# Performance work log

Measured on AMD Instinct MI355X. Metric: run time of the kernel, lower is better.

## Reference

```python
import jax, jax.numpy as jnp
import numpy as np

B, S, D, H, HID = 4, 1024, 1024, 16, 4096
DK = D // H
EPS = 1e-6


def _ln(x):
    # LayerNorm without affine, eps=1e-6
    mu = jnp.mean(x, axis=-1, keepdims=True)
    var = jnp.var(x, axis=-1, keepdims=True)
    return (x - mu) / jnp.sqrt(var + EPS)


def _lin(x, W, b):
    # torch Linear convention: W is [out, in]
    y = jnp.einsum('...i,oi->...o', x, W)
    return y + b if b is not None else y


def setup_inputs() -> dict:
    key = jax.random.key(0)
    ks = jax.random.split(key, 16)
    sc = lambda fan_in: 1.0 / np.sqrt(fan_in)
    inp = {
        'x': jax.random.normal(ks[0], (B, S, D), jnp.float32),
        'cond': jax.random.normal(ks[1], (B, 1, D), jnp.float32),
        'Wq': jax.random.normal(ks[2], (D, D), jnp.float32) * sc(D),
        'bq': jnp.zeros((D,), jnp.float32),
        'Wk': jax.random.normal(ks[3], (D, D), jnp.float32) * sc(D),
        'bk': jnp.zeros((D,), jnp.float32),
        'Wv': jax.random.normal(ks[4], (D, D), jnp.float32) * sc(D),
        'bv': jnp.zeros((D,), jnp.float32),
        'Wo': jax.random.normal(ks[5], (D, D), jnp.float32) * sc(D),
        'bo': jnp.zeros((D,), jnp.float32),
        'W1': jax.random.normal(ks[6], (HID, D), jnp.float32) * sc(D),
        'b1': jnp.zeros((HID,), jnp.float32),
        'W2': jax.random.normal(ks[7], (D, HID), jnp.float32) * sc(HID),
        'b2': jnp.zeros((D,), jnp.float32),
        'Wada': jax.random.normal(ks[8], (6 * D, D), jnp.float32) * sc(D),
        'bada': jnp.zeros((6 * D,), jnp.float32),
    }
    return inp


def reference(x, cond, Wq, bq, Wk, bk, Wv, bv, Wo, bo, W1, b1, W2, b2, Wada, bada):
    # adaLN modulation: SiLU -> Linear -> chunk 6 along last dim
    mod = _lin(jax.nn.silu(cond), Wada, bada)  # [B,1,6D]
    gama1, beta1, alpha1, gama2, beta2, alpha2 = jnp.split(mod, 6, axis=-1)

    # attention branch
    residual = x
    h = _ln(x) * (1.0 + beta1) + gama1  # modulate(shift=gama1, scale=beta1)
    q = _lin(h, Wq, bq).reshape(B, S, H, DK)
    k = _lin(h, Wk, bk).reshape(B, S, H, DK)
    v = _lin(h, Wv, bv).reshape(B, S, H, DK)
    scores = jnp.einsum('bqhd,bkhd->bhqk', q, k) / jnp.sqrt(jnp.float32(DK))
    probs = jax.nn.softmax(scores, axis=-1)
    attn = jnp.einsum('bhqk,bkhd->bqhd', probs, v).reshape(B, S, D)
    attn = _lin(attn, Wo, bo)
    x = residual + alpha1 * attn

    # MLP branch
    residual = x
    h = _ln(x) * (1.0 + beta2) + gama2
    h = _lin(h, W1, b1)
    h = jax.nn.gelu(h, approximate=False)  # torch nn.GELU default (erf)
    h = _lin(h, W2, b2)
    return residual + alpha2 * h
```

## Files before the change

### kernel.cpp

```cpp
#include <hip/hip_runtime.h>
#include <cstdint>

typedef __bf16 bf16_t;
typedef __bf16 bf16x4 __attribute__((ext_vector_type(4)));
typedef __bf16 bf16x8 __attribute__((ext_vector_type(8)));
typedef float f32x4 __attribute__((ext_vector_type(4)));

#define B_ 4
#define S_ 1024
#define D_ 1024
#define HID_ 4096
#define MEG (1u << 20)

static const size_t OFF_WBF  = 0;
static const size_t OFF_BQKV = 25165824;
static const size_t OFF_MOD  = 25178112;
static const size_t OFF_H    = 25276416;
static const size_t OFF_QKV  = 33665024;
static const size_t OFF_VT   = 58830848;
static const size_t OFF_ATTN = 67219456;
static const size_t OFF_X1   = 75608064;
static const size_t OFF_PART = 92385280;
static const size_t OFF_MLPH = 159494144;

__device__ __forceinline__ void async_copy16(const bf16_t* g, bf16_t* l) {
  __builtin_amdgcn_global_load_lds(
      (__attribute__((address_space(1))) void*)(g),
      (__attribute__((address_space(3))) void*)(l), 16, 0, 0);
}

__global__ __launch_bounds__(256) void convert_pack(
    const float* __restrict__ Wq, const float* __restrict__ Wk,
    const float* __restrict__ Wv, const float* __restrict__ Wo,
    const float* __restrict__ W1, const float* __restrict__ W2,
    const float* __restrict__ bq, const float* __restrict__ bk,
    const float* __restrict__ bv, bf16_t* __restrict__ wbf,
    float* __restrict__ bqkv) {
  const int y = blockIdx.y;
  if (y == 6) {
    int i = blockIdx.x * 256 + threadIdx.x;
    if (i < 3072)
      bqkv[i] = i < 1024 ? bq[i] : (i < 2048 ? bk[i - 1024] : bv[i - 2048]);
    return;
  }
  const float* src; bf16_t* dst; int n;
  switch (y) {
    case 0: src = Wq; dst = wbf;           n = MEG;     break;
    case 1: src = Wk; dst = wbf + MEG;     n = MEG;     break;
    case 2: src = Wv; dst = wbf + 2*MEG;   n = MEG;     break;
    case 3: src = Wo; dst = wbf + 3*MEG;   n = MEG;     break;
    case 4: src = W1; dst = wbf + 4*MEG;   n = 4*MEG;   break;
    default: src = W2; dst = wbf + 8*MEG;  n = 4*MEG;   break;
  }
  int idx = (blockIdx.x * 256 + threadIdx.x) * 4;
  if (idx < n) {
    float4 v = *(const float4*)(src + idx);
    bf16x4 pk;
    pk.x = (__bf16)v.x; pk.y = (__bf16)v.y; pk.z = (__bf16)v.z; pk.w = (__bf16)v.w;
    *(bf16x4*)(dst + idx) = pk;
  }
}

__global__ __launch_bounds__(256) void ada_mod(
    const float* __restrict__ cond, const float* __restrict__ Wada,
    const float* __restrict__ bada, float* __restrict__ mod) {
  const int wave = threadIdx.x >> 6, lane = threadIdx.x & 63;
  const int o = blockIdx.x * 4 + wave;
  const float* wr = Wada + (size_t)o * D_;
  float a0 = 0.f, a1 = 0.f, a2 = 0.f, a3 = 0.f;
#pragma unroll
  for (int l = 0; l < 16; l++) {
    int i = l * 64 + lane;
    float w = wr[i];
    float c0 = cond[i], c1 = cond[1024 + i], c2 = cond[2048 + i], c3 = cond[3072 + i];
    a0 += w * (c0 / (1.0f + __expf(-c0)));
    a1 += w * (c1 / (1.0f + __expf(-c1)));
    a2 += w * (c2 / (1.0f + __expf(-c2)));
    a3 += w * (c3 / (1.0f + __expf(-c3)));
  }
#pragma unroll
  for (int offs = 32; offs; offs >>= 1) {
    a0 += __shfl_xor(a0, offs);
    a1 += __shfl_xor(a1, offs);
    a2 += __shfl_xor(a2, offs);
    a3 += __shfl_xor(a3, offs);
  }
  if (lane == 0) {
    float bb = bada[o];
    mod[o]          = a0 + bb;
    mod[6144 + o]   = a1 + bb;
    mod[12288 + o]  = a2 + bb;
    mod[18432 + o]  = a3 + bb;
  }
}

__global__ __launch_bounds__(256) void ln_modulate(
    const float* __restrict__ X, const float* __restrict__ mod,
    bf16_t* __restrict__ H, int goff) {
  const int row = blockIdx.x;
  const int b = row >> 10;
  const int t = threadIdx.x;
  const float* xr = X + (size_t)row * D_;
  float4 xv = *(const float4*)(xr + t * 4);
  float s = xv.x + xv.y + xv.z + xv.w;
  float q = xv.x*xv.x + xv.y*xv.y + xv.z*xv.z + xv.w*xv.w;
  const int wave = t >> 6, lane = t & 63;
#pragma unroll
  for (int offs = 32; offs; offs >>= 1) {
    s += __shfl_down(s, offs);
    q += __shfl_down(q, offs);
  }
  __shared__ float sb[4][2];
  if (lane == 0) { sb[wave][0] = s; sb[wave][1] = q; }
  __syncthreads();
  float st = sb[0][0] + sb[1][0] + sb[2][0] + sb[3][0];
  float qt = sb[0][1] + sb[1][1] + sb[2][1] + sb[3][1];
  float mu = st * (1.0f / D_);
  float var = qt * (1.0f / D_) - mu * mu;
  float rstd = rsqrtf(var + 1e-6f);
  const float* mb = mod + (size_t)b * 6144 + goff;
  const int c = t * 4;
  float4 gm = *(const float4*)(mb + c);
  float4 bt = *(const float4*)(mb + 1024 + c);
  bf16x4 pk;
  pk.x = (__bf16)((xv.x - mu) * rstd * (1.0f + bt.x) + gm.x);
  pk.y = (__bf16)((xv.y - mu) * rstd * (1.0f + bt.y) + gm.y);
  pk.z = (__bf16)((xv.z - mu) * rstd * (1.0f + bt.z) + gm.z);
  pk.w = (__bf16)((xv.w - mu) * rstd * (1.0f + bt.w) + gm.w);
  *(bf16x4*)(H + (size_t)row * D_ + c) = pk;
}

__global__ __launch_bounds__(256) void transpose_v(
    const bf16_t* __restrict__ qkv, bf16_t* __restrict__ vT) {
  __shared__ bf16_t tile[64][65];
  const int bh = blockIdx.y;
  const int b = bh >> 4, hh = bh & 15;
  const int s0 = blockIdx.x * 64;
  const int t = threadIdx.x;
  const int tx = t & 63, ty = t >> 6;
  const bf16_t* src = qkv + (size_t)b * S_ * 3072 + 2048 + hh * 64;
  for (int r = ty; r < 64; r += 4)
    tile[r][tx] = src[(size_t)(s0 + r) * 3072 + tx];
  __syncthreads();
  bf16_t* dst = vT + (size_t)bh * 64 * 1024;
  for (int r = ty; r < 64; r += 4)
    dst[(size_t)r * 1024 + s0 + tx] = tile[tx][r];
}

__global__ __launch_bounds__(512, 4) void flash_attn(
    const bf16_t* __restrict__ qkv, const bf16_t* __restrict__ vT,
    bf16_t* __restrict__ attn) {
  __shared__ __align__(16) bf16_t Ks[2][2][64 * 64];
  __shared__ __align__(16) bf16_t Vs[2][2][64 * 64];
  __shared__ __align__(16) bf16_t Ps[8][16 * 64];

  const int t = threadIdx.x;
  const int wave = t >> 6, lane = t & 63;
  const int lm = lane & 15, quad = lane >> 4;
  const int bh = blockIdx.y;
  const int b = bh >> 4, hh = bh & 15;
  const int s0 = blockIdx.x * 128;

  const bf16_t* qbase = qkv + (size_t)b * S_ * 3072 + hh * 64;
  const bf16_t* kbase = qbase + 1024;
  const bf16_t* vbase = vT + (size_t)bh * (64 * 1024);

  const int row0 = t >> 3;
  const int cg = (t & 7) ^ (row0 & 7);
  const int od = t * 8;

  async_copy16(qbase + (size_t)(s0 + row0) * 3072 + cg * 8, &Ks[1][0][od]);
  async_copy16(qbase + (size_t)(s0 + 64 + row0) * 3072 + cg * 8, &Ks[1][1][od]);
  async_copy16(kbase + (size_t)row0 * 3072 + cg * 8, &Ks[0][0][od]);
  async_copy16(kbase + (size_t)(64 + row0) * 3072 + cg * 8, &Ks[0][1][od]);
  async_copy16(vbase + (size_t)row0 * 1024 + cg * 8, &Vs[0][0][od]);
  async_copy16(vbase + (size_t)row0 * 1024 + 64 + cg * 8, &Vs[0][1][od]);
  __syncthreads();

  bf16x8 aq0, aq1;
  {
    const int rq = wave * 16 + lm;
    const int qh = rq >> 6, qr = rq & 63;
    const int rbq = lm & 7;
    aq0 = *(const bf16x8*)&Ks[1][qh][qr * 64 + (quad ^ rbq) * 8];
    aq1 = *(const bf16x8*)&Ks[1][qh][qr * 64 + ((4 + quad) ^ rbq) * 8];
  }
  __syncthreads();

  f32x4 accO[4] = {};
  float mrow[4], lsum[4];
#pragma unroll
  for (int r = 0; r < 4; r++) { mrow[r] = -1e30f; lsum[r] = 0.f; }

  const float SC = 0.18033688f;
  const int rb = lm & 7;
  bf16_t* Pw = Ps[wave];

  for (int tt = 0; tt < 8; ++tt) {
    const int cur = tt & 1;
    if (tt < 7) {
      const int nb = cur ^ 1;
      const size_t k0n = (size_t)(tt + 1) << 7;
      async_copy16(kbase + (k0n + row0) * 3072 + cg * 8, &Ks[nb][0][od]);
      async_copy16(kbase + (k0n + 64 + row0) * 3072 + cg * 8, &Ks[nb][1][od]);
      async_copy16(vbase + (size_t)row0 * 1024 + k0n + cg * 8, &Vs[nb][0][od]);
      async_copy16(vbase + (size_t)row0 * 1024 + k0n + 64 + cg * 8, &Vs[nb][1][od]);
    }

    f32x4 accS[8];
#pragma unroll
    for (int j = 0; j < 8; j++) accS[j] = (f32x4){0.f, 0.f, 0.f, 0.f};
    __builtin_amdgcn_s_setprio(1);
#pragma unroll
    for (int hf = 0; hf < 2; hf++) {
#pragma unroll
      for (int ni = 0; ni < 4; ni++) {
        const int rk = ni * 16 + lm;
        bf16x8 b0 = *(const bf16x8*)&Ks[cur][hf][rk * 64 + ((quad ^ rb)) * 8];
        bf16x8 b1 = *(const bf16x8*)&Ks[cur][hf][rk * 64 + (((4 + quad) ^ rb)) * 8];
        f32x4 a = accS[hf * 4 + ni];
        a = __builtin_amdgcn_mfma_f32_16x16x32_bf16(aq0, b0, a, 0, 0, 0);
        a = __builtin_amdgcn_mfma_f32_16x16x32_bf16(aq1, b1, a, 0, 0, 0);
        accS[hf * 4 + ni] = a;
      }
    }
    __builtin_amdgcn_s_setprio(0);

    float mx[4];
#pragma unroll
    for (int r = 0; r < 4; r++) {
      float m0 = fmaxf(fmaxf(accS[0][r], accS[1][r]), fmaxf(accS[2][r], accS[3][r]));
      float m1 = fmaxf(fmaxf(accS[4][r], accS[5][r]), fmaxf(accS[6][r], accS[7][r]));
      float m8 = fmaxf(m0, m1);
      m8 = fmaxf(m8, __shfl_xor(m8, 1));
      m8 = fmaxf(m8, __shfl_xor(m8, 2));
      m8 = fmaxf(m8, __shfl_xor(m8, 4));
      m8 = fmaxf(m8, __shfl_xor(m8, 8));
      mx[r] = m8 * SC;
    }
    bool ok = (mx[0] - mrow[0] <= 8.0f) && (mx[1] - mrow[1] <= 8.0f) &&
              (mx[2] - mrow[2] <= 8.0f) && (mx[3] - mrow[3] <= 8.0f);
    if (!__all(ok)) {
#pragma unroll
      for (int r = 0; r < 4; r++) {
        float mnew = fmaxf(mrow[r], mx[r]);
        float al = exp2f(mrow[r] - mnew);
        mrow[r] = mnew;
        lsum[r] *= al;
#pragma unroll
        for (int di = 0; di < 4; di++) accO[di][r] *= al;
      }
    }
#pragma unroll
    for (int r = 0; r < 4; r++) {
      float sum = 0.f;
#pragma unroll
      for (int j = 0; j < 8; j++) {
        float p = exp2f(accS[j][r] * SC - mrow[r]);
        accS[j][r] = p;
        sum += p;
      }
      lsum[r] += sum;
    }

#pragma unroll
    for (int hf = 0; hf < 2; hf++) {
#pragma unroll
      for (int jj = 0; jj < 4; jj++)
#pragma unroll
        for (int r = 0; r < 4; r++) {
          int prow = quad * 4 + r;
          int c = jj * 16 + lm;
          Pw[prow * 64 + (((c >> 3) ^ (prow & 7)) << 3) + (c & 7)] =
              (__bf16)accS[hf * 4 + jj][r];
        }
      __builtin_amdgcn_s_setprio(1);
#pragma unroll
      for (int loc = 0; loc < 2; loc++) {
        bf16x8 ap = *(const bf16x8*)&Pw[lm * 64 + (((loc * 4 + quad) ^ rb)) * 8];
#pragma unroll
        for (int di = 0; di < 4; di++) {
          const int rv = di * 16 + lm;
          bf16x8 vv = *(const bf16x8*)&Vs[cur][hf]
              [rv * 64 + (((loc * 4 + quad) ^ rb)) * 8];
          accO[di] = __builtin_amdgcn_mfma_f32_16x16x32_bf16(ap, vv, accO[di], 0, 0, 0);
        }
      }
      __builtin_amdgcn_s_setprio(0);
    }
    __syncthreads();
  }

#pragma unroll
  for (int r = 0; r < 4; r++) {
    float sv = lsum[r];
    sv += __shfl_xor(sv, 1);
    sv += __shfl_xor(sv, 2);
    sv += __shfl_xor(sv, 4);
    sv += __shfl_xor(sv, 8);
    lsum[r] = sv;
  }

#pragma unroll
  for (int r = 0; r < 4; r++) {
    float inv = 1.0f / lsum[r];
    int prow = quad * 4 + r;
#pragma unroll
    for (int di = 0; di < 4; di++) {
      int col = di * 16 + lm;
      int cph = (col >> 3) ^ (prow & 7);
      Pw[prow * 64 + cph * 8 + (col & 7)] = (__bf16)(accO[di][r] * inv);
    }
  }
  bf16_t* abase = attn + (size_t)b * S_ * 1024 +
                  (size_t)(s0 + wave * 16) * 1024 + hh * 64;
#pragma unroll
  for (int it = 0; it < 2; it++) {
    int slot = it * 64 + lane;
    int orow = slot >> 3;
    int gc = slot & 7;
    int cph = gc ^ (orow & 7);
    bf16x8 val = *(const bf16x8*)&Pw[orow * 64 + cph * 8];
    *(bf16x8*)(abase + (size_t)orow * 1024 + gc * 8) = val;
  }
}

template <int EPI>
__global__ __launch_bounds__(512) void gemm_bt(
    const bf16_t* __restrict__ A, int lda, long long sAz,
    const bf16_t* __restrict__ B, int ldb, long long sBz,
    void* __restrict__ Cv, int ldc, long long sCz,
    int M, int N, int K,
    const float* __restrict__ bias,
    float scale) {
  __shared__ __align__(16) bf16_t As[3][256 * 64];
  __shared__ __align__(16) bf16_t Bs[3][128 * 64];

  const int z = blockIdx.z;
  A += (size_t)z * sAz;
  B += (size_t)z * sBz;

  const int gx = gridDim.x;
  int d = blockIdx.x + gx * blockIdx.y;
  {
    const int cpx = (gx * gridDim.y) >> 3;
    int wg = (d & 7) * cpx + (d >> 3);
    const int by = wg / gx;
    const int bx = wg % gx;

    const int t = threadIdx.x;
    const int wave = t >> 6;
    const int lane = t & 63;
    const int lm = lane & 15;
    const int quad = lane >> 4;
    const int wr = wave >> 1;
    const int wc = wave & 1;

    const int m0 = by * 256;
    const int n0 = bx * 128;

    f32x4 acc[4][4] = {};

    const int srow = t >> 3;
    const int scg = (t & 7) ^ (srow & 7);
    const int sod = t * 8;
    const bf16_t* Ag = A + (size_t)(m0 + srow) * lda + scg * 8;
    const bf16_t* Bg = B + (size_t)(n0 + srow) * ldb + scg * 8;
    const size_t a64 = (size_t)64 * lda, a128 = (size_t)128 * lda,
                 a192 = (size_t)192 * lda, b64 = (size_t)64 * ldb;

#define STAGE6(buf, ko)                                      \
  async_copy16(Ag + (ko), &As[buf][sod]);                    \
  async_copy16(Ag + a64 + (ko), &As[buf][4096 + sod]);       \
  async_copy16(Ag + a128 + (ko), &As[buf][8192 + sod]);      \
  async_copy16(Ag + a192 + (ko), &As[buf][12288 + sod]);     \
  async_copy16(Bg + (ko), &Bs[buf][sod]);                    \
  async_copy16(Bg + b64 + (ko), &Bs[buf][4096 + sod]);

    const int niter = K >> 6;
    STAGE6(0, 0);
    STAGE6(1, 64);

    const int rbx = lm & 7;
    const int sl0 = (quad ^ rbx) * 8;
    const int sl1 = ((4 + quad) ^ rbx) * 8;
    const int arow = wr * 4096 + lm * 64;
    const int brow = wc * 4096 + lm * 64;

    int cur = 0;
    for (int it = 0; it < niter; ++it) {
      if (it + 1 < niter) {
        asm volatile("s_waitcnt vmcnt(6)\n\ts_barrier" ::: "memory");
      } else {
        asm volatile("s_waitcnt vmcnt(0)\n\ts_barrier" ::: "memory");
      }
      if (it + 2 < niter) {
        const int nb = (cur >= 1) ? cur - 1 : 2;
        const int ko = (it + 2) << 6;
        STAGE6(nb, ko);
      }
      bf16x8 af[4][2], bfr[4][2];
#pragma unroll
      for (int i = 0; i < 4; i++) {
        af[i][0] = *(const bf16x8*)&As[cur][arow + i * 1024 + sl0];
        af[i][1] = *(const bf16x8*)&As[cur][arow + i * 1024 + sl1];
        bfr[i][0] = *(const bf16x8*)&Bs[cur][brow + i * 1024 + sl0];
        bfr[i][1] = *(const bf16x8*)&Bs[cur][brow + i * 1024 + sl1];
      }
      __builtin_amdgcn_s_setprio(1);
#pragma unroll
      for (int ks = 0; ks < 2; ks++)
#pragma unroll
        for (int mi = 0; mi < 4; mi++)
#pragma unroll
          for (int ni = 0; ni < 4; ni++)
            acc[mi][ni] = __builtin_amdgcn_mfma_f32_16x16x32_bf16(
                af[mi][ks], bfr[ni][ks], acc[mi][ni], 0, 0, 0);
      __builtin_amdgcn_s_setprio(0);
      cur = (cur == 2) ? 0 : cur + 1;
    }
#undef STAGE6

    const size_t cz = (size_t)z * sCz;
#pragma unroll
    for (int mi = 0; mi < 4; mi++) {
#pragma unroll
      for (int ni = 0; ni < 4; ni++) {
#pragma unroll
        for (int r = 0; r < 4; r++) {
          int row = m0 + wr * 64 + mi * 16 + quad * 4 + r;
          int col = n0 + wc * 64 + ni * 16 + lm;
          float v = acc[mi][ni][r];
          size_t idx = cz + (size_t)row * ldc + col;
          if (EPI == 1) {
            ((float*)Cv)[idx] = v * scale;
          } else if (EPI == 0) {
            if (bias) v += bias[col];
            ((bf16_t*)Cv)[idx] = (__bf16)v;
          } else if (EPI == 3) {
            v += bias[col];
            float u = 1.5957691216f * (v + 0.044715f * v * v * v);
            float g = v / (1.0f + __expf(-u));
            ((bf16_t*)Cv)[idx] = (__bf16)g;
          }
        }
      }
    }
  }
}

__global__ __launch_bounds__(256) void reduce_ln(
    const float* __restrict__ part, const float* __restrict__ x,
    const float* __restrict__ bo, const float* __restrict__ mod,
    float* __restrict__ x1, bf16_t* __restrict__ h) {
  const int row = blockIdx.x;
  const int b = row >> 10;
  const int t = threadIdx.x;
  const int c = t * 4;
  const size_t idx = (size_t)row * 1024 + c;
  float4 p0 = *(const float4*)(part + idx);
  float4 p1 = *(const float4*)(part + 4194304 + idx);
  float4 bb = *(const float4*)(bo + c);
  float4 al = *(const float4*)(mod + (size_t)b * 6144 + 2048 + c);
  float4 xs = *(const float4*)(x + idx);
  float4 xv;
  xv.x = xs.x + al.x * (p0.x + p1.x + bb.x);
  xv.y = xs.y + al.y * (p0.y + p1.y + bb.y);
  xv.z = xs.z + al.z * (p0.z + p1.z + bb.z);
  xv.w = xs.w + al.w * (p0.w + p1.w + bb.w);
  *(float4*)(x1 + idx) = xv;

  float s = xv.x + xv.y + xv.z + xv.w;
  float q = xv.x*xv.x + xv.y*xv.y + xv.z*xv.z + xv.w*xv.w;
  const int wave = t >> 6, lane = t & 63;
#pragma unroll
  for (int offs = 32; offs; offs >>= 1) {
    s += __shfl_down(s, offs);
    q += __shfl_down(q, offs);
  }
  __shared__ float sb[4][2];
  if (lane == 0) { sb[wave][0] = s; sb[wave][1] = q; }
  __syncthreads();
  float st = sb[0][0] + sb[1][0] + sb[2][0] + sb[3][0];
  float qt = sb[0][1] + sb[1][1] + sb[2][1] + sb[3][1];
  float mu = st * (1.0f / D_);
  float var = qt * (1.0f / D_) - mu * mu;
  float rstd = rsqrtf(var + 1e-6f);
  const float* mb = mod + (size_t)b * 6144 + 3072;
  float4 gm = *(const float4*)(mb + c);
  float4 bt = *(const float4*)(mb + 1024 + c);
  bf16x4 pk;
  pk.x = (__bf16)((xv.x - mu) * rstd * (1.0f + bt.x) + gm.x);
  pk.y = (__bf16)((xv.y - mu) * rstd * (1.0f + bt.y) + gm.y);
  pk.z = (__bf16)((xv.z - mu) * rstd * (1.0f + bt.z) + gm.z);
  pk.w = (__bf16)((xv.w - mu) * rstd * (1.0f + bt.w) + gm.w);
  *(bf16x4*)(h + idx) = pk;
}

__global__ __launch_bounds__(256) void reduce_w2(
    const float* __restrict__ part, const float* __restrict__ x1,
    const float* __restrict__ b2, const float* __restrict__ mod,
    float* __restrict__ out) {
  const int idx = (blockIdx.x * 256 + threadIdx.x) * 4;
  const int col = idx & 1023;
  const int row = idx >> 10;
  const int b = row >> 10;
  float4 s0 = *(const float4*)(part + idx);
  float4 s1 = *(const float4*)(part + 4194304 + idx);
  float4 bb = *(const float4*)(b2 + col);
  float4 al = *(const float4*)(mod + (size_t)b * 6144 + 5120 + col);
  float4 rs = *(const float4*)(x1 + idx);
  float4 o;
  o.x = rs.x + al.x * (s0.x + s1.x + bb.x);
  o.y = rs.y + al.y * (s0.y + s1.y + bb.y);
  o.z = rs.z + al.z * (s0.z + s1.z + bb.z);
  o.w = rs.w + al.w * (s0.w + s1.w + bb.w);
  *(float4*)(out + idx) = o;
}

extern "C" void kernel_launch(void* const* d_in, const int* in_sizes, int n_in,
                              void* d_out, int out_size, void* d_ws, size_t ws_size,
                              hipStream_t stream) {
  (void)in_sizes; (void)n_in; (void)out_size; (void)ws_size;
  const float* x    = (const float*)d_in[0];
  const float* cond = (const float*)d_in[1];
  const float* Wq   = (const float*)d_in[2];
  const float* bq   = (const float*)d_in[3];
  const float* Wk   = (const float*)d_in[4];
  const float* bk   = (const float*)d_in[5];
  const float* Wv   = (const float*)d_in[6];
  const float* bv   = (const float*)d_in[7];
  const float* Wo   = (const float*)d_in[8];
  const float* bo   = (const float*)d_in[9];
  const float* W1   = (const float*)d_in[10];
  const float* b1   = (const float*)d_in[11];
  const float* W2   = (const float*)d_in[12];
  const float* b2   = (const float*)d_in[13];
  const float* Wada = (const float*)d_in[14];
  const float* bada = (const float*)d_in[15];

  uint8_t* ws = (uint8_t*)d_ws;
  bf16_t* wbf   = (bf16_t*)(ws + OFF_WBF);
  float*  bqkv  = (float*)(ws + OFF_BQKV);
  float*  mod   = (float*)(ws + OFF_MOD);
  bf16_t* h     = (bf16_t*)(ws + OFF_H);
  bf16_t* qkv   = (bf16_t*)(ws + OFF_QKV);
  bf16_t* vT    = (bf16_t*)(ws + OFF_VT);
  bf16_t* attn  = (bf16_t*)(ws + OFF_ATTN);
  float*  x1    = (float*)(ws + OFF_X1);
  float*  part  = (float*)(ws + OFF_PART);
  bf16_t* mlph  = (bf16_t*)(ws + OFF_MLPH);
  float* out = (float*)d_out;

  convert_pack<<<dim3(4096, 7, 1), 256, 0, stream>>>(Wq, Wk, Wv, Wo, W1, W2,
                                                     bq, bk, bv, wbf, bqkv);
  ada_mod<<<1536, 256, 0, stream>>>(cond, Wada, bada, mod);
  ln_modulate<<<4096, 256, 0, stream>>>(x, mod, h, 0);
  gemm_bt<0><<<dim3(24, 16, 1), 512, 0, stream>>>(
      h, 1024, 0, wbf, 1024, 0, qkv, 3072, 0, 4096, 3072, 1024,
      bqkv, 1.f);
  transpose_v<<<dim3(16, 64, 1), 256, 0, stream>>>(qkv, vT);
  flash_attn<<<dim3(8, 64, 1), 512, 0, stream>>>(qkv, vT, attn);

  gemm_bt<1><<<dim3(8, 16, 2), 512, 0, stream>>>(
      attn, 1024, 512, wbf + (size_t)3 * MEG, 1024, 512, part, 1024, 4194304,
      4096, 1024, 512, nullptr, 1.f);
  reduce_ln<<<4096, 256, 0, stream>>>(part, x, bo, mod, x1, h);

  gemm_bt<3><<<dim3(32, 16, 1), 512, 0, stream>>>(
      h, 1024, 0, wbf + (size_t)4 * MEG, 1024, 0, mlph, 4096, 0,
      4096, 4096, 1024, b1, 1.f);
  gemm_bt<1><<<dim3(8, 16, 2), 512, 0, stream>>>(
      mlph, 4096, 2048, wbf + (size_t)8 * MEG, 4096, 2048, part, 1024, 4194304,
      4096, 1024, 2048, nullptr, 1.f);
  reduce_w2<<<4096, 256, 0, stream>>>(part, x1, b2, mod, out);
}
```

Baseline: 412.5 us.

## Split GEMM main loop into two phases interleaving LDS reads, async copies and MFMAs

Each K-iteration of the bf16 GEMM main loop now runs in two halves. Each half reads part of the A fragments from LDS, issues half of the next-stage async global-to-LDS copies, and runs half of the MFMAs, with extra barriers between phases. The goal is to overlap global loads and LDS traffic with matrix-core work more finely, in a ping-pong style schedule. The cost is four barriers per iteration instead of one, and a possible change in register pressure.

```diff
diff --git a/kernel.cpp b/kernel.cpp
--- a/kernel.cpp
+++ b/kernel.cpp
@@ -390,32 +390,65 @@
     int cur = 0;
     for (int it = 0; it < niter; ++it) {
       if (it + 1 < niter) {
-        asm volatile("s_waitcnt vmcnt(6)\n\ts_barrier" ::: "memory");
+        asm volatile("s_waitcnt vmcnt(6)" ::: "memory");
       } else {
-        asm volatile("s_waitcnt vmcnt(0)\n\ts_barrier" ::: "memory");
-      }
-      if (it + 2 < niter) {
-        const int nb = (cur >= 1) ? cur - 1 : 2;
-        const int ko = (it + 2) << 6;
-        STAGE6(nb, ko);
-      }
-      bf16x8 af[4][2], bfr[4][2];
+        asm volatile("s_waitcnt vmcnt(0)" ::: "memory");
+      }
+      __builtin_amdgcn_s_barrier();
+      const int nb = (cur >= 1) ? cur - 1 : 2;
+      const int ko = (it + 2) << 6;
+      const bool st = (it + 2 < niter);
+
+      bf16x8 af0[2], af1[2], bfr[4][2];
+      af0[0] = *(const bf16x8*)&As[cur][arow + sl0];
+      af0[1] = *(const bf16x8*)&As[cur][arow + sl1];
+      af1[0] = *(const bf16x8*)&As[cur][arow + 1024 + sl0];
+      af1[1] = *(const bf16x8*)&As[cur][arow + 1024 + sl1];
 #pragma unroll
       for (int i = 0; i < 4; i++) {
-        af[i][0] = *(const bf16x8*)&As[cur][arow + i * 1024 + sl0];
-        af[i][1] = *(const bf16x8*)&As[cur][arow + i * 1024 + sl1];
         bfr[i][0] = *(const bf16x8*)&Bs[cur][brow + i * 1024 + sl0];
         bfr[i][1] = *(const bf16x8*)&Bs[cur][brow + i * 1024 + sl1];
       }
+      if (st) {
+        async_copy16(Ag + ko, &As[nb][sod]);
+        async_copy16(Ag + a64 + ko, &As[nb][4096 + sod]);
+        async_copy16(Ag + a128 + ko, &As[nb][8192 + sod]);
+      }
+      __builtin_amdgcn_s_barrier();
       __builtin_amdgcn_s_setprio(1);
 #pragma unroll
       for (int ks = 0; ks < 2; ks++)
 #pragma unroll
-        for (int mi = 0; mi < 4; mi++)
-#pragma unroll
-          for (int ni = 0; ni < 4; ni++)
-            acc[mi][ni] = __builtin_amdgcn_mfma_f32_16x16x32_bf16(
-                af[mi][ks], bfr[ni][ks], acc[mi][ni], 0, 0, 0);
+        for (int ni = 0; ni < 4; ni++) {
+          acc[0][ni] = __builtin_amdgcn_mfma_f32_16x16x32_bf16(
+              af0[ks], bfr[ni][ks], acc[0][ni], 0, 0, 0);
+          acc[1][ni] = __builtin_amdgcn_mfma_f32_16x16x32_bf16(
+              af1[ks], bfr[ni][ks], acc[1][ni], 0, 0, 0);
+        }
+      __builtin_amdgcn_s_setprio(0);
+      __builtin_amdgcn_s_barrier();
+
+      bf16x8 af2[2], af3[2];
+      af2[0] = *(const bf16x8*)&As[cur][arow + 2048 + sl0];
+      af2[1] = *(const bf16x8*)&As[cur][arow + 2048 + sl1];
+      af3[0] = *(const bf16x8*)&As[cur][arow + 3072 + sl0];
+      af3[1] = *(const bf16x8*)&As[cur][arow + 3072 + sl1];
+      if (st) {
+        async_copy16(Ag + a192 + ko, &As[nb][12288 + sod]);
+        async_copy16(Bg + ko, &Bs[nb][sod]);
+        async_copy16(Bg + b64 + ko, &Bs[nb][4096 + sod]);
+      }
+      __builtin_amdgcn_s_barrier();
+      __builtin_amdgcn_s_setprio(1);
+#pragma unroll
+      for (int ks = 0; ks < 2; ks++)
+#pragma unroll
+        for (int ni = 0; ni < 4; ni++) {
+          acc[2][ni] = __builtin_amdgcn_mfma_f32_16x16x32_bf16(
+              af2[ks], bfr[ni][ks], acc[2][ni], 0, 0, 0);
+          acc[3][ni] = __builtin_amdgcn_mfma_f32_16x16x32_bf16(
+              af3[ks], bfr[ni][ks], acc[3][ni], 0, 0, 0);
+        }
       __builtin_amdgcn_s_setprio(0);
       cur = (cur == 2) ? 0 : cur + 1;
     }
```

Measured after the change: 390.8 us. 5.3% less time.
